# Performance work log

Hardware: AMD Instinct MI355X
Metric: run time of the kernel (lower is better)

The kernel has to match this reference:

```python
import jax, jax.numpy as jnp
import numpy as np

N_NODES = 10000
N_EDGES = 640000
IN_DIM, HID_DIM, OUT_DIM = 128, 512, 512


def setup_inputs() -> dict:
    key = jax.random.key(0)
    k1, k2, k3, k4, k5, k6 = jax.random.split(key, 6)
    feat = jax.random.normal(k1, (N_NODES, IN_DIM), dtype=jnp.float32)
    edge_index = jax.random.randint(k2, (2, N_EDGES), 0, N_NODES, dtype=jnp.int64)
    s1 = 1.0 / np.sqrt(IN_DIM)
    s2 = 1.0 / np.sqrt(HID_DIM)
    W1 = jax.random.uniform(k3, (IN_DIM, HID_DIM), jnp.float32, -s1, s1)
    b1 = jnp.zeros((HID_DIM,), jnp.float32)
    W2 = jax.random.uniform(k4, (HID_DIM, OUT_DIM), jnp.float32, -s2, s2)
    b2 = jnp.zeros((OUT_DIM,), jnp.float32)
    return {"feat": feat, "edge_index": edge_index, "W1": W1, "b1": b1, "W2": W2, "b2": b2}


def _degree_norms(edge_index, n_nodes):
    src, dst = edge_index[0], edge_index[1]
    ones = jnp.ones((edge_index.shape[1],), jnp.float32)
    out_deg = jax.ops.segment_sum(ones, src, num_segments=n_nodes)
    in_deg = jax.ops.segment_sum(ones, dst, num_segments=n_nodes)
    # DGL clamps degree to >= 1 to avoid division by zero
    norm_src = jax.lax.rsqrt(jnp.maximum(out_deg, 1.0))  # [N]
    norm_dst = jax.lax.rsqrt(jnp.maximum(in_deg, 1.0))   # [N]
    return norm_src, norm_dst


def _graph_conv(x, src, dst, norm_src, norm_dst, W, b, n_nodes):
    # norm='both': D_in^{-1/2} A D_out^{-1/2} X W + b
    x = x * norm_src[:, None]
    agg = jax.ops.segment_sum(x[src], dst, num_segments=n_nodes)  # [N, d]
    agg = agg * norm_dst[:, None]
    return agg @ W + b


def reference(feat, edge_index, W1, b1, W2, b2):
    n = feat.shape[0]
    src, dst = edge_index[0], edge_index[1]
    norm_src, norm_dst = _degree_norms(edge_index, n)
    h = _graph_conv(feat, src, dst, norm_src, norm_dst, W1, b1, n)
    h = jax.nn.relu(h)
    out = _graph_conv(h, src, dst, norm_src, norm_dst, W2, b2, n)
    return out
```

## Files before the change

kernel.cpp:

```cpp
#include <hip/hip_runtime.h>

#define NN 10000
#define NE 640000
#define IN_DIM 128
#define HID_DIM 512
#define OUT_DIM 512
#define NB 10240
#define P_PART 128
#define EPB (NE / P_PART)

typedef __attribute__((ext_vector_type(8))) short short8;
typedef __attribute__((ext_vector_type(4))) float f32x4;
typedef __attribute__((ext_vector_type(2))) float f32x2;

__device__ __forceinline__ ushort f2b(float f) {
    union { float f; uint i; } c; c.f = f;
    uint x = c.i;
    uint r = (x + 0x7fffu + ((x >> 16) & 1u)) >> 16;
    return (ushort)r;
}
__device__ __forceinline__ float blo(uint a) {
    union { uint i; float f; } c; c.i = a << 16; return c.f;
}
__device__ __forceinline__ float bhi(uint a) {
    union { uint i; float f; } c; c.i = a & 0xffff0000u; return c.f;
}

__device__ __forceinline__ void gl_lds16(const ushort* g, ushort* l) {
    __builtin_amdgcn_global_load_lds((const __attribute__((address_space(1))) uint*)g,
                                     (__attribute__((address_space(3))) uint*)l, 16, 0, 0);
}

__global__ __launch_bounds__(1024) void histw_kernel(const int* __restrict__ ei,
                                                     ushort* __restrict__ pcnt_dst,
                                                     ushort* __restrict__ pcnt_src,
                                                     const float* __restrict__ W1,
                                                     ushort* __restrict__ W1t,
                                                     const float* __restrict__ W2,
                                                     ushort* __restrict__ W2t) {
    __shared__ int h[NB];
    int b = blockIdx.x;
    int t = threadIdx.x;
    if (b < 256) {
        int p = b & 127;
        const int* __restrict__ idx = (b < 128) ? (ei + NE) : ei;
        ushort* __restrict__ outp = (b < 128) ? pcnt_dst : pcnt_src;
        for (int i = t; i < NB; i += 1024) h[i] = 0;
        __syncthreads();
        int base = p * EPB;
        for (int i = t; i < EPB; i += 1024) atomicAdd(&h[idx[base + i]], 1);
        __syncthreads();
        for (int i = t; i < NB; i += 1024) outp[p * NB + i] = (ushort)h[i];
        return;
    }
    float* tld = (float*)h;
    const float* W; ushort* Wt; int K, N, k0, n0;
    if (b < 320) {
        int bb = b - 256;
        W = W1; Wt = W1t; K = IN_DIM; N = HID_DIM;
        k0 = (bb & 3) * 32; n0 = (bb >> 2) * 32;
    } else {
        int bb = b - 320;
        W = W2; Wt = W2t; K = HID_DIM; N = OUT_DIM;
        k0 = (bb & 15) * 32; n0 = (bb >> 4) * 32;
    }
    int r = t >> 5, c = t & 31;
    tld[r * 33 + c] = W[(size_t)(k0 + r) * N + n0 + c];
    __syncthreads();
    Wt[(size_t)(n0 + r) * K + k0 + c] = f2b(tld[c * 33 + r]);
}

__global__ __launch_bounds__(256) void colreduce_kernel(const ushort* __restrict__ pcnt_dst,
                                                        const ushort* __restrict__ pcnt_src,
                                                        int* __restrict__ poff,
                                                        int* __restrict__ deg_in,
                                                        float* __restrict__ norm_src,
                                                        float* __restrict__ norm_dst) {
    int v = blockIdx.x * 256 + threadIdx.x;
    int s = 0;
#pragma unroll 4
    for (int p = 0; p < P_PART; p++) {
        int c = pcnt_dst[p * NB + v];
        poff[p * NB + v] = s;
        s += c;
    }
    deg_in[v] = s;
    int s2 = 0;
#pragma unroll 4
    for (int p = 0; p < P_PART; p++) s2 += pcnt_src[p * NB + v];
    if (v < NN) {
        norm_dst[v] = rsqrtf(fmaxf((float)s, 1.0f));
        norm_src[v] = rsqrtf(fmaxf((float)s2, 1.0f));
    }
}

__global__ __launch_bounds__(1024) void scanfeat_kernel(const int* __restrict__ deg,
                                                        int* __restrict__ row_off,
                                                        const float* __restrict__ feat,
                                                        const float* __restrict__ norm_src,
                                                        ushort* __restrict__ featb) {
    int b = blockIdx.x;
    int t = threadIdx.x;
    if (b == 0) {
        const int PER = NB / 1024;
        __shared__ int lds[1024];
        int base = t * PER;
        int local[PER];
        int s = 0;
#pragma unroll
        for (int i = 0; i < PER; i++) {
            int v = deg[base + i];
            local[i] = s;
            s += v;
        }
        lds[t] = s;
        __syncthreads();
        for (int off = 1; off < 1024; off <<= 1) {
            int x = (t >= off) ? lds[t - off] : 0;
            __syncthreads();
            lds[t] += x;
            __syncthreads();
        }
        int excl = lds[t] - s;
#pragma unroll
        for (int i = 0; i < PER; i++) {
            int idx = base + i;
            if (idx <= NN) row_off[idx] = excl + local[i];
        }
        return;
    }
    int i = (b - 1) * 1024 + t;
    if (i < NN * IN_DIM / 4) {
        float4 v = ((const float4*)feat)[i];
        float s = norm_src[i >> 5];
        ushort4 o;
        o.x = f2b(v.x * s); o.y = f2b(v.y * s); o.z = f2b(v.z * s); o.w = f2b(v.w * s);
        ((ushort4*)featb)[i] = o;
    }
}

__global__ __launch_bounds__(1024) void fill_kernel(const int* __restrict__ src,
                                                    const int* __restrict__ dst,
                                                    const int* __restrict__ row_off,
                                                    const int* __restrict__ poff,
                                                    int* __restrict__ csr_src) {
    __shared__ int cur[NB];
    int p = blockIdx.x, t = threadIdx.x;
    for (int i = t; i < NB; i += 1024)
        cur[i] = ((i < NN) ? row_off[i] : 0) + poff[p * NB + i];
    __syncthreads();
    int base = p * EPB;
    for (int i = t; i < EPB; i += 1024) {
        int d = dst[base + i];
        int slot = atomicAdd(&cur[d], 1);
        csr_src[slot] = src[base + i];
    }
}

__global__ __launch_bounds__(64) void agg1_kernel(const uint* __restrict__ fb,
                                                  const int* __restrict__ row_off,
                                                  const int* __restrict__ csr_src,
                                                  const float* __restrict__ norm_dst,
                                                  uint* __restrict__ aggb) {
    int node = blockIdx.x;
    uint lane = threadIdx.x;
    int beg = row_off[node], end = row_off[node + 1];
    f32x2 acc = {0.f, 0.f};
    int i = beg;
    for (; i + 8 <= end; i += 8) {
        const uint* rp[8];
#pragma unroll
        for (int j = 0; j < 8; j++)
            rp[j] = fb + (uint)__builtin_amdgcn_readfirstlane(csr_src[i + j]) * 64u;
        uint a[8];
#pragma unroll
        for (int j = 0; j < 8; j++) a[j] = rp[j][lane];
#pragma unroll
        for (int j = 0; j < 8; j++) {
            f32x2 v; v.x = blo(a[j]); v.y = bhi(a[j]);
            acc += v;
        }
    }
    for (; i < end; i++) {
        const uint* rp = fb + (uint)__builtin_amdgcn_readfirstlane(csr_src[i]) * 64u;
        uint a = rp[lane];
        f32x2 v; v.x = blo(a); v.y = bhi(a);
        acc += v;
    }
    float nd = norm_dst[node];
    aggb[node * 64 + lane] = (uint)f2b(acc.x * nd) | ((uint)f2b(acc.y * nd) << 16);
}

__global__ __launch_bounds__(64) void agg2_kernel(const uint* __restrict__ hb,
                                                  const int* __restrict__ row_off,
                                                  const int* __restrict__ csr_src,
                                                  const float* __restrict__ norm_dst,
                                                  uint* __restrict__ aggb) {
    uint b = blockIdx.x;
    uint xcd = b & 7u;
    int node = (int)((b >> 3) * 2u + (xcd >> 2));
    uint t = (xcd & 3u) * 64u + threadIdx.x;
    int beg = row_off[node], end = row_off[node + 1];
    f32x2 acc = {0.f, 0.f};
    int i = beg;
    for (; i + 8 <= end; i += 8) {
        const uint* rp[8];
#pragma unroll
        for (int j = 0; j < 8; j++)
            rp[j] = hb + (uint)__builtin_amdgcn_readfirstlane(csr_src[i + j]) * 256u;
        uint a[8];
#pragma unroll
        for (int j = 0; j < 8; j++) a[j] = rp[j][t];
#pragma unroll
        for (int j = 0; j < 8; j++) {
            f32x2 v; v.x = blo(a[j]); v.y = bhi(a[j]);
            acc += v;
        }
    }
    for (; i < end; i++) {
        const uint* rp = hb + (uint)__builtin_amdgcn_readfirstlane(csr_src[i]) * 256u;
        uint a = rp[t];
        f32x2 v; v.x = blo(a); v.y = bhi(a);
        acc += v;
    }
    float nd = norm_dst[node];
    aggb[(uint)node * 256u + t] = (uint)f2b(acc.x * nd) | ((uint)f2b(acc.y * nd) << 16);
}

template <int EPI>
__global__ __launch_bounds__(256) void gemm_bf16_kernel(const ushort* __restrict__ A,
                                                        const ushort* __restrict__ Bt,
                                                        const float* __restrict__ bias,
                                                        const float* __restrict__ scale,
                                                        void* __restrict__ Cout,
                                                        int M, int K, int N) {
    __shared__ __align__(16) ushort As[2][128 * 32];
    __shared__ __align__(16) ushort Bs[2][128 * 32];
    int tid = threadIdx.x;
    int lane = tid & 63;
    int wid = tid >> 6;
    int bm = blockIdx.x * 128;
    int bn = blockIdx.y * 128;
    int wm = (wid & 1) * 64;
    int wn = (wid >> 1) * 64;

    int c0 = tid, c1 = 256 + tid;
    int row0 = ((c0 >> 6) << 4) | (c0 & 15), kq0 = (c0 >> 4) & 3;
    int row1 = ((c1 >> 6) << 4) | (c1 & 15), kq1 = (c1 >> 4) & 3;
    const ushort* sA0 = A + (size_t)(bm + row0) * K + kq0 * 8;
    const ushort* sA1 = A + (size_t)(bm + row1) * K + kq1 * 8;
    const ushort* sB0 = Bt + (size_t)(bn + row0) * K + kq0 * 8;
    const ushort* sB1 = Bt + (size_t)(bn + row1) * K + kq1 * 8;
    uint lo0 = (uint)(wid * 64) * 8u;
    uint lo1 = (uint)(256 + wid * 64) * 8u;

    f32x4 acc[4][4] = {};

    const int NT = K / 32;
    gl_lds16(sA0, &As[0][lo0]);
    gl_lds16(sA1, &As[0][lo1]);
    gl_lds16(sB0, &Bs[0][lo0]);
    gl_lds16(sB1, &Bs[0][lo1]);
    __syncthreads();

    int cur = 0;
    for (int t = 0; t < NT; t++) {
        if (t + 1 < NT) {
            int kn = (t + 1) * 32;
            gl_lds16(sA0 + kn, &As[cur ^ 1][lo0]);
            gl_lds16(sA1 + kn, &As[cur ^ 1][lo1]);
            gl_lds16(sB0 + kn, &Bs[cur ^ 1][lo0]);
            gl_lds16(sB1 + kn, &Bs[cur ^ 1][lo1]);
        }
        short8 af[4], bfr[4];
        int fo = ((lane >> 4) << 4) + (lane & 15);
#pragma unroll
        for (int i = 0; i < 4; i++) {
            int j = (((wm >> 4) + i) << 6) + fo;
            af[i] = *(const short8*)(&As[cur][j * 8]);
        }
#pragma unroll
        for (int i = 0; i < 4; i++) {
            int j = (((wn >> 4) + i) << 6) + fo;
            bfr[i] = *(const short8*)(&Bs[cur][j * 8]);
        }
#pragma unroll
        for (int i = 0; i < 4; i++)
#pragma unroll
            for (int jn = 0; jn < 4; jn++)
                acc[i][jn] = __builtin_amdgcn_mfma_f32_16x16x32_bf16(af[i], bfr[jn], acc[i][jn], 0, 0, 0);
        if (t + 1 < NT) {
            __syncthreads();
            cur ^= 1;
        }
    }

#pragma unroll
    for (int i = 0; i < 4; i++) {
#pragma unroll
        for (int jn = 0; jn < 4; jn++) {
            int col = bn + wn + jn * 16 + (lane & 15);
            float bv = bias[col];
#pragma unroll
            for (int r = 0; r < 4; r++) {
                int gm = bm + wm + i * 16 + ((lane >> 4) << 2) + r;
                if (gm < M) {
                    float v = acc[i][jn][r] + bv;
                    if (EPI == 1) {
                        v = fmaxf(v, 0.f) * scale[gm];
                        ((ushort*)Cout)[(size_t)gm * N + col] = f2b(v);
                    } else {
                        ((float*)Cout)[(size_t)gm * N + col] = v;
                    }
                }
            }
        }
    }
}

extern "C" void kernel_launch(void* const* d_in, const int* in_sizes, int n_in,
                              void* d_out, int out_size, void* d_ws, size_t ws_size,
                              hipStream_t stream) {
    const float* feat = (const float*)d_in[0];
    const int* ei = (const int*)d_in[1];
    const float* W1 = (const float*)d_in[2];
    const float* b1 = (const float*)d_in[3];
    const float* W2 = (const float*)d_in[4];
    const float* b2 = (const float*)d_in[5];
    float* out = (float*)d_out;

    const int* src = ei;
    const int* dst = ei + NE;
    const int NNP = 10112;

    char* ws = (char*)d_ws;
    size_t off = 0;
    auto alloc = [&](size_t bytes) -> void* {
        void* p = ws + off;
        off += (bytes + 255) & ~(size_t)255;
        return p;
    };
    int* row_off = (int*)alloc((NN + 16) * sizeof(int));
    int* deg_in = (int*)alloc(NB * sizeof(int));
    float* norm_src = (float*)alloc(NN * sizeof(float));
    float* norm_dst = (float*)alloc(NN * sizeof(float));
    int* csr_src = (int*)alloc(NE * sizeof(int));
    ushort* featb = (ushort*)alloc((size_t)NN * IN_DIM * 2);
    ushort* W1t = (ushort*)alloc((size_t)HID_DIM * IN_DIM * 2);
    ushort* W2t = (ushort*)alloc((size_t)OUT_DIM * HID_DIM * 2);
    size_t union_base = off;
    ushort* pcnt_dst = (ushort*)alloc((size_t)P_PART * NB * sizeof(ushort));
    ushort* pcnt_src = (ushort*)alloc((size_t)P_PART * NB * sizeof(ushort));
    int* poff = (int*)alloc((size_t)P_PART * NB * sizeof(int));
    off = union_base;
    ushort* agg1b = (ushort*)alloc((size_t)NNP * IN_DIM * 2);
    ushort* hb = (ushort*)alloc((size_t)NN * HID_DIM * 2);
    ushort* agg2b = (ushort*)alloc((size_t)NNP * HID_DIM * 2);

    histw_kernel<<<576, 1024, 0, stream>>>(ei, pcnt_dst, pcnt_src, W1, W1t, W2, W2t);
    colreduce_kernel<<<NB / 256, 256, 0, stream>>>(pcnt_dst, pcnt_src, poff, deg_in, norm_src, norm_dst);
    scanfeat_kernel<<<314, 1024, 0, stream>>>(deg_in, row_off, feat, norm_src, featb);
    fill_kernel<<<P_PART, 1024, 0, stream>>>(src, dst, row_off, poff, csr_src);

    agg1_kernel<<<NN, 64, 0, stream>>>((const uint*)featb, row_off, csr_src, norm_dst, (uint*)agg1b);
    {
        dim3 grid(NNP / 128, HID_DIM / 128);
        gemm_bf16_kernel<1><<<grid, 256, 0, stream>>>(agg1b, W1t, b1, norm_src, hb, NN, IN_DIM, HID_DIM);
    }
    agg2_kernel<<<NN / 2 * 8, 64, 0, stream>>>((const uint*)hb, row_off, csr_src, norm_dst, (uint*)agg2b);
    {
        dim3 grid(NNP / 128, OUT_DIM / 128);
        gemm_bf16_kernel<0><<<grid, 256, 0, stream>>>(agg2b, W2t, b2, nullptr, out, NN, HID_DIM, OUT_DIM);
    }
}
```

Measured before the change: 132.8 us.

## Fold scan into fill, move feat cast into hist, batch CSR index loads

Removes the separate scan/feature-cast kernel. The bf16 cast of feat moves into the histogram kernel, and the norm_src scaling is now applied per edge inside agg1. Each fill block recomputes the degree prefix scan redundantly, and block 0 writes row_off. The aggregation kernels load 64 CSR indices per wave in one vector load and broadcast them with readlane, replacing 8 scalar readfirstlane loads per step. This saves a launch and scalar load latency, at the cost of redundant scans in 128 blocks and extra norm_src gathers in agg1.

New measurement: 143.1 us. +7.8%, slower.

```diff
diff --git a/kernel.cpp b/kernel.cpp
--- a/kernel.cpp
+++ b/kernel.cpp
@@ -31,13 +31,15 @@
                                      (__attribute__((address_space(3))) uint*)l, 16, 0, 0);
 }
 
-__global__ __launch_bounds__(1024) void histw_kernel(const int* __restrict__ ei,
-                                                     ushort* __restrict__ pcnt_dst,
-                                                     ushort* __restrict__ pcnt_src,
-                                                     const float* __restrict__ W1,
-                                                     ushort* __restrict__ W1t,
-                                                     const float* __restrict__ W2,
-                                                     ushort* __restrict__ W2t) {
+__global__ __launch_bounds__(1024) void histwf_kernel(const int* __restrict__ ei,
+                                                      ushort* __restrict__ pcnt_dst,
+                                                      ushort* __restrict__ pcnt_src,
+                                                      const float* __restrict__ W1,
+                                                      ushort* __restrict__ W1t,
+                                                      const float* __restrict__ W2,
+                                                      ushort* __restrict__ W2t,
+                                                      const float* __restrict__ feat,
+                                                      ushort* __restrict__ featb) {
     __shared__ int h[NB];
     int b = blockIdx.x;
     int t = threadIdx.x;
@@ -53,6 +55,16 @@
         for (int i = t; i < NB; i += 1024) outp[p * NB + i] = (ushort)h[i];
         return;
     }
+    if (b >= 576) {
+        int i = (b - 576) * 1024 + t;
+        if (i < NN * IN_DIM / 4) {
+            float4 v = ((const float4*)feat)[i];
+            ushort4 o;
+            o.x = f2b(v.x); o.y = f2b(v.y); o.z = f2b(v.z); o.w = f2b(v.w);
+            ((ushort4*)featb)[i] = o;
+        }
+        return;
+    }
     float* tld = (float*)h;
     const float* W; ushort* Wt; int K, N, k0, n0;
     if (b < 320) {
@@ -94,72 +106,54 @@
     }
 }
 
-__global__ __launch_bounds__(1024) void scanfeat_kernel(const int* __restrict__ deg,
-                                                        int* __restrict__ row_off,
-                                                        const float* __restrict__ feat,
-                                                        const float* __restrict__ norm_src,
-                                                        ushort* __restrict__ featb) {
-    int b = blockIdx.x;
-    int t = threadIdx.x;
-    if (b == 0) {
-        const int PER = NB / 1024;
-        __shared__ int lds[1024];
-        int base = t * PER;
-        int local[PER];
-        int s = 0;
-#pragma unroll
-        for (int i = 0; i < PER; i++) {
-            int v = deg[base + i];
-            local[i] = s;
-            s += v;
-        }
-        lds[t] = s;
-        __syncthreads();
-        for (int off = 1; off < 1024; off <<= 1) {
-            int x = (t >= off) ? lds[t - off] : 0;
-            __syncthreads();
-            lds[t] += x;
-            __syncthreads();
-        }
-        int excl = lds[t] - s;
-#pragma unroll
-        for (int i = 0; i < PER; i++) {
-            int idx = base + i;
-            if (idx <= NN) row_off[idx] = excl + local[i];
-        }
-        return;
-    }
-    int i = (b - 1) * 1024 + t;
-    if (i < NN * IN_DIM / 4) {
-        float4 v = ((const float4*)feat)[i];
-        float s = norm_src[i >> 5];
-        ushort4 o;
-        o.x = f2b(v.x * s); o.y = f2b(v.y * s); o.z = f2b(v.z * s); o.w = f2b(v.w * s);
-        ((ushort4*)featb)[i] = o;
-    }
-}
-
 __global__ __launch_bounds__(1024) void fill_kernel(const int* __restrict__ src,
                                                     const int* __restrict__ dst,
-                                                    const int* __restrict__ row_off,
+                                                    const int* __restrict__ deg_in,
                                                     const int* __restrict__ poff,
+                                                    int* __restrict__ row_off,
                                                     int* __restrict__ csr_src) {
     __shared__ int cur[NB];
+    __shared__ int lds[1024];
     int p = blockIdx.x, t = threadIdx.x;
-    for (int i = t; i < NB; i += 1024)
-        cur[i] = ((i < NN) ? row_off[i] : 0) + poff[p * NB + i];
+    const int PER = NB / 1024;
+    int base = t * PER;
+    int local[PER];
+    int s = 0;
+#pragma unroll
+    for (int i = 0; i < PER; i++) {
+        int v = deg_in[base + i];
+        local[i] = s;
+        s += v;
+    }
+    lds[t] = s;
     __syncthreads();
-    int base = p * EPB;
+    for (int off = 1; off < 1024; off <<= 1) {
+        int x = (t >= off) ? lds[t - off] : 0;
+        __syncthreads();
+        lds[t] += x;
+        __syncthreads();
+    }
+    int excl = lds[t] - s;
+#pragma unroll
+    for (int i = 0; i < PER; i++) {
+        int idx = base + i;
+        int ro = excl + local[i];
+        cur[idx] = ro + poff[p * NB + idx];
+        if (p == 0 && idx <= NN) row_off[idx] = ro;
+    }
+    __syncthreads();
+    int ebase = p * EPB;
     for (int i = t; i < EPB; i += 1024) {
-        int d = dst[base + i];
+        int d = dst[ebase + i];
         int slot = atomicAdd(&cur[d], 1);
-        csr_src[slot] = src[base + i];
+        csr_src[slot] = src[ebase + i];
     }
 }
 
 __global__ __launch_bounds__(64) void agg1_kernel(const uint* __restrict__ fb,
                                                   const int* __restrict__ row_off,
                                                   const int* __restrict__ csr_src,
+                                                  const float* __restrict__ norm_src,
                                                   const float* __restrict__ norm_dst,
                                                   uint* __restrict__ aggb) {
     int node = blockIdx.x;
@@ -167,25 +161,37 @@
     int beg = row_off[node], end = row_off[node + 1];
     f32x2 acc = {0.f, 0.f};
     int i = beg;
+    int bb = beg;
+    uint idxv = 0;
+    if (i + 8 <= end) idxv = (uint)csr_src[min(bb + (int)lane, end - 1)];
     for (; i + 8 <= end; i += 8) {
-        const uint* rp[8];
-#pragma unroll
-        for (int j = 0; j < 8; j++)
-            rp[j] = fb + (uint)__builtin_amdgcn_readfirstlane(csr_src[i + j]) * 64u;
+        int o = i - bb;
+        if (o >= 64) {
+            bb = i;
+            idxv = (uint)csr_src[min(bb + (int)lane, end - 1)];
+            o = 0;
+        }
+        uint u[8];
+#pragma unroll
+        for (int j = 0; j < 8; j++) u[j] = (uint)__builtin_amdgcn_readlane((int)idxv, o + j);
         uint a[8];
 #pragma unroll
-        for (int j = 0; j < 8; j++) a[j] = rp[j][lane];
+        for (int j = 0; j < 8; j++) a[j] = fb[u[j] * 64u + lane];
+        float ns[8];
+#pragma unroll
+        for (int j = 0; j < 8; j++) ns[j] = norm_src[u[j]];
 #pragma unroll
         for (int j = 0; j < 8; j++) {
-            f32x2 v; v.x = blo(a[j]); v.y = bhi(a[j]);
-            acc += v;
+            acc.x += blo(a[j]) * ns[j];
+            acc.y += bhi(a[j]) * ns[j];
         }
     }
     for (; i < end; i++) {
-        const uint* rp = fb + (uint)__builtin_amdgcn_readfirstlane(csr_src[i]) * 64u;
-        uint a = rp[lane];
-        f32x2 v; v.x = blo(a); v.y = bhi(a);
-        acc += v;
+        uint u = (uint)__builtin_amdgcn_readfirstlane(csr_src[i]);
+        uint a = fb[u * 64u + lane];
+        float ns = norm_src[u];
+        acc.x += blo(a) * ns;
+        acc.y += bhi(a) * ns;
     }
     float nd = norm_dst[node];
     aggb[node * 64 + lane] = (uint)f2b(acc.x * nd) | ((uint)f2b(acc.y * nd) << 16);
@@ -203,14 +209,22 @@
     int beg = row_off[node], end = row_off[node + 1];
     f32x2 acc = {0.f, 0.f};
     int i = beg;
+    int bb = beg;
+    uint idxv = 0;
+    if (i + 8 <= end) idxv = (uint)csr_src[min(bb + (int)threadIdx.x, end - 1)];
     for (; i + 8 <= end; i += 8) {
-        const uint* rp[8];
-#pragma unroll
-        for (int j = 0; j < 8; j++)
-            rp[j] = hb + (uint)__builtin_amdgcn_readfirstlane(csr_src[i + j]) * 256u;
+        int o = i - bb;
+        if (o >= 64) {
+            bb = i;
+            idxv = (uint)csr_src[min(bb + (int)threadIdx.x, end - 1)];
+            o = 0;
+        }
+        uint u[8];
+#pragma unroll
+        for (int j = 0; j < 8; j++) u[j] = (uint)__builtin_amdgcn_readlane((int)idxv, o + j);
         uint a[8];
 #pragma unroll
-        for (int j = 0; j < 8; j++) a[j] = rp[j][t];
+        for (int j = 0; j < 8; j++) a[j] = hb[u[j] * 256u + t];
 #pragma unroll
         for (int j = 0; j < 8; j++) {
             f32x2 v; v.x = blo(a[j]); v.y = bhi(a[j]);
@@ -218,8 +232,8 @@
         }
     }
     for (; i < end; i++) {
-        const uint* rp = hb + (uint)__builtin_amdgcn_readfirstlane(csr_src[i]) * 256u;
-        uint a = rp[t];
+        uint u = (uint)__builtin_amdgcn_readfirstlane(csr_src[i]);
+        uint a = hb[u * 256u + t];
         f32x2 v; v.x = blo(a); v.y = bhi(a);
         acc += v;
     }
@@ -357,12 +371,11 @@
     ushort* hb = (ushort*)alloc((size_t)NN * HID_DIM * 2);
     ushort* agg2b = (ushort*)alloc((size_t)NNP * HID_DIM * 2);
 
-    histw_kernel<<<576, 1024, 0, stream>>>(ei, pcnt_dst, pcnt_src, W1, W1t, W2, W2t);
+    histwf_kernel<<<889, 1024, 0, stream>>>(ei, pcnt_dst, pcnt_src, W1, W1t, W2, W2t, feat, featb);
     colreduce_kernel<<<NB / 256, 256, 0, stream>>>(pcnt_dst, pcnt_src, poff, deg_in, norm_src, norm_dst);
-    scanfeat_kernel<<<314, 1024, 0, stream>>>(deg_in, row_off, feat, norm_src, featb);
-    fill_kernel<<<P_PART, 1024, 0, stream>>>(src, dst, row_off, poff, csr_src);
-
-    agg1_kernel<<<NN, 64, 0, stream>>>((const uint*)featb, row_off, csr_src, norm_dst, (uint*)agg1b);
+    fill_kernel<<<P_PART, 1024, 0, stream>>>(src, dst, deg_in, poff, row_off, csr_src);
+
+    agg1_kernel<<<NN, 64, 0, stream>>>((const uint*)featb, row_off, csr_src, norm_src, norm_dst, (uint*)agg1b);
     {
         dim3 grid(NNP / 128, HID_DIM / 128);
         gemm_bf16_kernel<1><<<grid, 256, 0, stream>>>(agg1b, W1t, b1, norm_src, hb, NN, IN_DIM, HID_DIM);
```
